# Optimization experiments

Measured on AMD Instinct MI355X. Metric: run time of the kernel, lower is better.

Reference implementation:

```python
import jax, jax.numpy as jnp
import numpy as np

N = 50000          # nodes
E = 600000         # edges
D_IN = 256         # input_feat_dim
H1 = 128           # hidden_dim1
H2 = 64            # hidden_dim2
DK = 64            # trs_depth (total key/value depth)
HEADS = 2


def setup_inputs() -> dict:
    key = jax.random.key(0)
    ks = jax.random.split(key, 12)
    inp = {
        "ns_emb": jax.random.normal(ks[0], (N, D_IN), dtype=jnp.float32),
        "edge_rows": jax.random.randint(ks[1], (E,), 0, N, dtype=jnp.int32),
        "edge_cols": jax.random.randint(ks[2], (E,), 0, N, dtype=jnp.int32),
        "edge_vals": jax.random.uniform(ks[3], (E,), dtype=jnp.float32),
        "condition": jax.random.normal(ks[4], (1, 128, H1), dtype=jnp.float32),
        # GCN linear weights (bias=False), stored [in, out]
        "W_hidden": jax.random.normal(ks[5], (D_IN, H1), dtype=jnp.float32) / np.sqrt(D_IN),
        "W_mu": jax.random.normal(ks[6], (H1, H2), dtype=jnp.float32) / np.sqrt(H1),
        "W_var": jax.random.normal(ks[7], (H1, H2), dtype=jnp.float32) / np.sqrt(H1),
        # MultiHeadAttention (bias-free) projections
        "Wq": jax.random.normal(ks[8], (H1, DK), dtype=jnp.float32) / np.sqrt(H1),
        "Wk": jax.random.normal(ks[9], (H1, DK), dtype=jnp.float32) / np.sqrt(H1),
        "Wv": jax.random.normal(ks[10], (H1, DK), dtype=jnp.float32) / np.sqrt(H1),
        "Wo": jax.random.normal(ks[11], (DK, H1), dtype=jnp.float32) / np.sqrt(DK),
    }
    return inp


def _spmm(rows, cols, vals, x):
    # sparse [N,N] @ x  via gather + segment-sum over COO edges
    gathered = vals[:, None] * x[cols]            # [E, d]
    return jax.ops.segment_sum(gathered, rows, num_segments=N)


def _gcn(x, W, rows, cols, vals):
    # dropout is identity in eval mode
    support = jax.nn.leaky_relu(x @ W)            # [N, out]
    out = _spmm(rows, cols, vals, support)        # [N, out]
    return jax.nn.leaky_relu(out)


def _mha(q, kv, Wq, Wk, Wv, Wo):
    # MoEL-style MultiHeadAttention, bias-free, no mask/dropout
    B, Lq, _ = q.shape
    Lk = kv.shape[1]
    dk = DK // HEADS
    Q = (q @ Wq).reshape(B, Lq, HEADS, dk).transpose(0, 2, 1, 3) * (dk ** -0.5)
    K = (kv @ Wk).reshape(B, Lk, HEADS, dk).transpose(0, 2, 1, 3)
    V = (kv @ Wv).reshape(B, Lk, HEADS, dk).transpose(0, 2, 1, 3)
    logits = jnp.einsum("bhqd,bhkd->bhqk", Q, K)
    w = jax.nn.softmax(logits, axis=-1)
    ctx = jnp.einsum("bhqk,bhkd->bhqd", w, V)
    ctx = ctx.transpose(0, 2, 1, 3).reshape(B, Lq, DK)
    return ctx @ Wo, w


def reference(ns_emb, edge_rows, edge_cols, edge_vals, condition,
              W_hidden, W_mu, W_var, Wq, Wk, Wv, Wo):
    hidden = _gcn(ns_emb, W_hidden, edge_rows, edge_cols, edge_vals)   # [N, H1]
    attended, _ = _mha(hidden[None], condition, Wq, Wk, Wv, Wo)        # [1, N, H1]
    h = attended[0]
    mu = _gcn(h, W_mu, edge_rows, edge_cols, edge_vals)                # [N, H2]
    var = _gcn(h, W_var, edge_rows, edge_cols, edge_vals)              # [N, H2]
    return mu, var
```

## Files before the change

### kernel.cpp

```cpp
#include <hip/hip_runtime.h>
#include <hip/hip_bf16.h>
#include <cstdint>


typedef __attribute__((ext_vector_type(8))) short short8;
typedef __attribute__((ext_vector_type(4))) float f32x4;
typedef __attribute__((ext_vector_type(4))) unsigned short ushort4_t;

__device__ __forceinline__ unsigned short f2bf(float f) {
    unsigned int u = __builtin_bit_cast(unsigned int, f);
    u += 0x7fffu + ((u >> 16) & 1u);
    return (unsigned short)(u >> 16);
}
__device__ __forceinline__ float bf2f(unsigned short v) {
    return __builtin_bit_cast(float, (unsigned int)v << 16);
}


__global__ void hist_kernel(const int* __restrict__ rows, int* __restrict__ cnt, int E) {
    int i = blockIdx.x * blockDim.x + threadIdx.x;
    if (i < E) atomicAdd(&cnt[rows[i]], 1);
}

__global__ void scan1_kernel(const int* __restrict__ cnt, int* __restrict__ excl,
                             int* __restrict__ bsum, int N) {
    __shared__ int sh[256];
    int t = threadIdx.x;
    int i = blockIdx.x * 256 + t;
    int v = (i < N) ? cnt[i] : 0;
    sh[t] = v;
    __syncthreads();
    for (int off = 1; off < 256; off <<= 1) {
        int x = (t >= off) ? sh[t - off] : 0;
        __syncthreads();
        sh[t] += x;
        __syncthreads();
    }
    if (i < N) excl[i] = sh[t] - v;
    if (t == 255) bsum[blockIdx.x] = sh[255];
}

__global__ void scan23_kernel(const int* __restrict__ excl, const int* __restrict__ bsum,
                              int* __restrict__ row_start, int* __restrict__ cursor,
                              int nb, int N, int E) {
    __shared__ int sh[256];
    int t = threadIdx.x;
    int v = (t < nb) ? bsum[t] : 0;
    sh[t] = v;
    __syncthreads();
    for (int off = 1; off < 256; off <<= 1) {
        int x = (t >= off) ? sh[t - off] : 0;
        __syncthreads();
        sh[t] += x;
        __syncthreads();
    }
    int boff = (blockIdx.x > 0) ? sh[blockIdx.x - 1] : 0;
    int i = blockIdx.x * 256 + t;
    if (i < N) {
        int w = excl[i] + boff;
        row_start[i] = w;
        cursor[i] = w;
    }
    if (i == 0) row_start[N] = E;
}

__global__ void scatter_kernel(const int* __restrict__ rows, const int* __restrict__ colsIn,
                               const float* __restrict__ valsIn, int* __restrict__ cursor,
                               int2* __restrict__ pack, int E) {
    int i = blockIdx.x * blockDim.x + threadIdx.x;
    if (i < E) {
        int r = rows[i];
        int p = atomicAdd(&cursor[r], 1);
        pack[p] = make_int2(colsIn[i], __float_as_int(valsIn[i]));
    }
}


__global__ __launch_bounds__(256) void prep_kv_kernel(
    const float* __restrict__ Wh, const float* __restrict__ Wq,
    const float* __restrict__ cond,
    const float* __restrict__ Wk, const float* __restrict__ Wv,
    const float* __restrict__ Wo, const float* __restrict__ Wmu,
    const float* __restrict__ Wvar,
    unsigned short* __restrict__ WhT, unsigned short* __restrict__ WqT,
    unsigned short* __restrict__ Ktt, unsigned short* __restrict__ Vt,
    unsigned short* __restrict__ WomT)
{
    const int t = threadIdx.x;
    const int bid = blockIdx.x;
    if (bid < 160) {
        int idx = bid * 256 + t;
        if (idx < 32768) {
            int n = idx & 127, k = idx >> 7;
            WhT[n * 256 + k] = f2bf(Wh[k * 128 + n]);
        } else {
            int i = idx - 32768, n = i & 63, k = i >> 6;
            WqT[n * 128 + k] = f2bf(Wq[k * 64 + n]);
        }
    } else if (bid < 224) {
        int b2 = bid - 160;
        __shared__ float c[2][128];
        c[t >> 7][t & 127] = cond[b2 * 256 + t];
        __syncthreads();
        int j = b2 * 2 + (t >> 7);
        int tl = t & 127;
        const float* W = (tl < 64) ? Wk : Wv;
        int col = tl & 63;
        float acc = 0.f;
#pragma unroll 8
        for (int k = 0; k < 128; ++k) acc = fmaf(c[t >> 7][k], W[k * 64 + col], acc);
        int h = col >> 5, d = col & 31;
        if (tl < 64) Ktt[((size_t)h * 128 + j) * 32 + d] = f2bf(acc * 0.17677669529663687f);
        else         Vt[((size_t)h * 32 + d) * 128 + j] = f2bf(acc);
    } else {
        int wb = bid - 224;
        __shared__ float WoTl[128 * 65];
#pragma unroll
        for (int i = 0; i < 32; ++i) {
            int idx = t + 256 * i;
            int d = idx >> 7, k = idx & 127;
            WoTl[k * 65 + d] = Wo[idx];
        }
        __syncthreads();
        int o = wb * 256 + t;
        int d = o & 63, n = o >> 6;
        const float* W = (n < 64) ? Wmu : Wvar;
        int j = n & 63;
        float acc = 0.f;
#pragma unroll 8
        for (int k = 0; k < 128; ++k) acc = fmaf(WoTl[k * 65 + d], W[k * 64 + j], acc);
        WomT[n * 64 + d] = f2bf(acc);
    }
}


__global__ __launch_bounds__(256) void gcn1_gemm(
    const float* __restrict__ A, const unsigned short* __restrict__ BT,
    unsigned short* __restrict__ C, int M)
{
    __shared__ unsigned short As[128][72];
    __shared__ unsigned short Bs[128][72];

    const int tid = threadIdx.x;
    const int lane = tid & 63, wave = tid >> 6;
    const int wm = wave & 1, wn = wave >> 1;
    const int quad = lane >> 4, l16 = lane & 15;
    const int r0 = blockIdx.x * 128;

    f32x4 acc[4][4];
#pragma unroll
    for (int mt = 0; mt < 4; ++mt)
#pragma unroll
        for (int nt = 0; nt < 4; ++nt)
#pragma unroll
            for (int r = 0; r < 4; ++r) acc[mt][nt][r] = 0.f;

    for (int kc = 0; kc < 256; kc += 64) {
#pragma unroll
        for (int i = 0; i < 8; ++i) {
            int f = tid + 256 * i;
            int row = f >> 4, kq = (f & 15) << 2;
            int gr = r0 + row;
            if (gr >= M) gr = M - 1;
            float4 v = *reinterpret_cast<const float4*>(&A[(size_t)gr * 256 + kc + kq]);
            unsigned int lo, hi;
            asm("v_cvt_pk_bf16_f32 %0, %1, %2" : "=v"(lo) : "v"(v.x), "v"(v.y));
            asm("v_cvt_pk_bf16_f32 %0, %1, %2" : "=v"(hi) : "v"(v.z), "v"(v.w));
            *reinterpret_cast<uint2*>(&As[row][kq]) = make_uint2(lo, hi);
        }
#pragma unroll
        for (int i = 0; i < 4; ++i) {
            int f = tid + 256 * i;
            int n = f >> 3, k8 = (f & 7) << 3;
            *reinterpret_cast<short8*>(&Bs[n][k8]) =
                *reinterpret_cast<const short8*>(&BT[(size_t)n * 256 + kc + k8]);
        }
        __syncthreads();

#pragma unroll
        for (int ks = 0; ks < 2; ++ks) {
            const int koff = ks * 32 + quad * 8;
            short8 a[4], b[4];
#pragma unroll
            for (int mt = 0; mt < 4; ++mt)
                a[mt] = *reinterpret_cast<const short8*>(&As[wm * 64 + mt * 16 + l16][koff]);
#pragma unroll
            for (int nt = 0; nt < 4; ++nt)
                b[nt] = *reinterpret_cast<const short8*>(&Bs[wn * 64 + nt * 16 + l16][koff]);
#pragma unroll
            for (int mt = 0; mt < 4; ++mt)
#pragma unroll
                for (int nt = 0; nt < 4; ++nt)
                    acc[mt][nt] = __builtin_amdgcn_mfma_f32_16x16x32_bf16(
                        a[mt], b[nt], acc[mt][nt], 0, 0, 0);
        }
        __syncthreads();
    }

#pragma unroll
    for (int mt = 0; mt < 4; ++mt)
#pragma unroll
        for (int nt = 0; nt < 4; ++nt) {
            int gc = wn * 64 + nt * 16 + l16;
#pragma unroll
            for (int r = 0; r < 4; ++r) {
                int gr = r0 + wm * 64 + mt * 16 + quad * 4 + r;
                if (gr < M) {
                    float v = acc[mt][nt][r];
                    v = v > 0.f ? v : 0.01f * v;
                    C[(size_t)gr * 128 + gc] = f2bf(v);
                }
            }
        }
}


__global__ __launch_bounds__(256) void attn_muvar_kernel(
    const unsigned short* __restrict__ hidden,
    const unsigned short* __restrict__ WqT,
    const unsigned short* __restrict__ Ktt,
    const unsigned short* __restrict__ Vt,
    const unsigned short* __restrict__ WomT,
    unsigned short* __restrict__ muvar,
    int M)
{
    __shared__ unsigned short Ap[64 * 136];
    __shared__ unsigned short Bp[10240];
    __shared__ unsigned short Cp[64 * 72];
    __shared__ float redm[2][64];
    __shared__ float reds[2][64];

    const int tid = threadIdx.x;
    const int lane = tid & 63, wave = tid >> 6;
    const int wm = wave & 1, wn = wave >> 1;
    const int quad = lane >> 4, l16 = lane & 15;
    const int r0 = blockIdx.x * 64;

#pragma unroll
    for (int i = 0; i < 4; ++i) {
        int f = tid + 256 * i;
        int row = f >> 4, k8 = (f & 15) << 3;
        int gr = r0 + row;
        if (gr >= M) gr = M - 1;
        *reinterpret_cast<short8*>(&Ap[row * 136 + k8]) =
            *reinterpret_cast<const short8*>(&hidden[(size_t)gr * 128 + k8]);
    }
#pragma unroll
    for (int i = 0; i < 4; ++i) {
        int f = tid + 256 * i;
        int n = f >> 4, k8 = (f & 15) << 3;
        *reinterpret_cast<short8*>(&Bp[n * 136 + k8]) =
            *reinterpret_cast<const short8*>(&WqT[(size_t)n * 128 + k8]);
    }
    __syncthreads();

    {
        f32x4 accq[2][2];
#pragma unroll
        for (int mt = 0; mt < 2; ++mt)
#pragma unroll
            for (int nt = 0; nt < 2; ++nt)
#pragma unroll
                for (int r = 0; r < 4; ++r) accq[mt][nt][r] = 0.f;
#pragma unroll
        for (int ks = 0; ks < 4; ++ks) {
            const int koff = ks * 32 + quad * 8;
            short8 a[2], b[2];
#pragma unroll
            for (int mt = 0; mt < 2; ++mt)
                a[mt] = *reinterpret_cast<const short8*>(&Ap[(wm * 32 + mt * 16 + l16) * 136 + koff]);
#pragma unroll
            for (int nt = 0; nt < 2; ++nt)
                b[nt] = *reinterpret_cast<const short8*>(&Bp[(wn * 32 + nt * 16 + l16) * 136 + koff]);
#pragma unroll
            for (int mt = 0; mt < 2; ++mt)
#pragma unroll
                for (int nt = 0; nt < 2; ++nt)
                    accq[mt][nt] = __builtin_amdgcn_mfma_f32_16x16x32_bf16(
                        a[mt], b[nt], accq[mt][nt], 0, 0, 0);
        }
#pragma unroll
        for (int mt = 0; mt < 2; ++mt)
#pragma unroll
            for (int nt = 0; nt < 2; ++nt) {
                int col = wn * 32 + nt * 16 + l16;
#pragma unroll
                for (int r = 0; r < 4; ++r) {
                    int row = wm * 32 + mt * 16 + quad * 4 + r;
                    Cp[row * 72 + col] = f2bf(accq[mt][nt][r]);
                }
            }
    }
    __syncthreads();

    for (int h = 0; h < 2; ++h) {
#pragma unroll
        for (int i = 0; i < 2; ++i) {
            int f = tid + 256 * i;
            int key = f >> 2, d8 = (f & 3) << 3;
            *reinterpret_cast<short8*>(&Bp[key * 40 + d8]) =
                *reinterpret_cast<const short8*>(&Ktt[((size_t)h * 128 + key) * 32 + d8]);
        }
#pragma unroll
        for (int i = 0; i < 2; ++i) {
            int f = tid + 256 * i;
            int d = f >> 4, k8 = (f & 15) << 3;
            *reinterpret_cast<short8*>(&Bp[5120 + d * 136 + k8]) =
                *reinterpret_cast<const short8*>(&Vt[((size_t)h * 32 + d) * 128 + k8]);
        }
        __syncthreads();

        f32x4 accl[2][4];
        {
            short8 a[2], b[4];
#pragma unroll
            for (int mt = 0; mt < 2; ++mt)
                a[mt] = *reinterpret_cast<const short8*>(&Cp[(wm * 32 + mt * 16 + l16) * 72 + h * 32 + quad * 8]);
#pragma unroll
            for (int nt = 0; nt < 4; ++nt)
                b[nt] = *reinterpret_cast<const short8*>(&Bp[(wn * 64 + nt * 16 + l16) * 40 + quad * 8]);
#pragma unroll
            for (int mt = 0; mt < 2; ++mt)
#pragma unroll
                for (int nt = 0; nt < 4; ++nt) {
                    f32x4 z; z[0] = 0.f; z[1] = 0.f; z[2] = 0.f; z[3] = 0.f;
                    accl[mt][nt] = __builtin_amdgcn_mfma_f32_16x16x32_bf16(a[mt], b[nt], z, 0, 0, 0);
                }
        }

#pragma unroll
        for (int mt = 0; mt < 2; ++mt)
#pragma unroll
            for (int r = 0; r < 4; ++r) {
                float mx = fmaxf(fmaxf(accl[mt][0][r], accl[mt][1][r]),
                                 fmaxf(accl[mt][2][r], accl[mt][3][r]));
#pragma unroll
                for (int off = 1; off < 16; off <<= 1)
                    mx = fmaxf(mx, __shfl_xor(mx, off, 64));
                if (l16 == 0) redm[wn][wm * 32 + mt * 16 + quad * 4 + r] = mx;
            }
        __syncthreads();
#pragma unroll
        for (int mt = 0; mt < 2; ++mt)
#pragma unroll
            for (int r = 0; r < 4; ++r) {
                int lr = wm * 32 + mt * 16 + quad * 4 + r;
                float fm = fmaxf(redm[0][lr], redm[1][lr]);
                float s = 0.f;
#pragma unroll
                for (int nt = 0; nt < 4; ++nt) {
                    float e = __expf(accl[mt][nt][r] - fm);
                    accl[mt][nt][r] = e;
                    s += e;
                }
#pragma unroll
                for (int off = 1; off < 16; off <<= 1)
                    s += __shfl_xor(s, off, 64);
                if (l16 == 0) reds[wn][lr] = s;
            }
        __syncthreads();
#pragma unroll
        for (int mt = 0; mt < 2; ++mt)
#pragma unroll
            for (int r = 0; r < 4; ++r) {
                int lr = wm * 32 + mt * 16 + quad * 4 + r;
                float inv = 1.0f / (reds[0][lr] + reds[1][lr]);
#pragma unroll
                for (int nt = 0; nt < 4; ++nt)
                    Ap[lr * 136 + wn * 64 + nt * 16 + l16] = f2bf(accl[mt][nt][r] * inv);
            }
        __syncthreads();

        {
            f32x4 accc[2];
#pragma unroll
            for (int mt = 0; mt < 2; ++mt)
#pragma unroll
                for (int r = 0; r < 4; ++r) accc[mt][r] = 0.f;
#pragma unroll
            for (int ks = 0; ks < 4; ++ks) {
                const int koff = ks * 32 + quad * 8;
                short8 a[2];
#pragma unroll
                for (int mt = 0; mt < 2; ++mt)
                    a[mt] = *reinterpret_cast<const short8*>(&Ap[(wm * 32 + mt * 16 + l16) * 136 + koff]);
                short8 bb = *reinterpret_cast<const short8*>(&Bp[5120 + (wn * 16 + l16) * 136 + koff]);
#pragma unroll
                for (int mt = 0; mt < 2; ++mt)
                    accc[mt] = __builtin_amdgcn_mfma_f32_16x16x32_bf16(a[mt], bb, accc[mt], 0, 0, 0);
            }
#pragma unroll
            for (int mt = 0; mt < 2; ++mt)
#pragma unroll
                for (int r = 0; r < 4; ++r) {
                    int row = wm * 32 + mt * 16 + quad * 4 + r;
                    Cp[row * 72 + h * 32 + wn * 16 + l16] = f2bf(accc[mt][r]);
                }
        }
        __syncthreads();
    }

#pragma unroll
    for (int i = 0; i < 4; ++i) {
        int f = tid + 256 * i;
        int n = f >> 3, k8 = (f & 7) << 3;
        *reinterpret_cast<short8*>(&Bp[n * 72 + k8]) =
            *reinterpret_cast<const short8*>(&WomT[(size_t)n * 64 + k8]);
    }
    __syncthreads();
    {
        f32x4 accf[2][4];
#pragma unroll
        for (int mt = 0; mt < 2; ++mt)
#pragma unroll
            for (int nt = 0; nt < 4; ++nt)
#pragma unroll
                for (int r = 0; r < 4; ++r) accf[mt][nt][r] = 0.f;
#pragma unroll
        for (int ks = 0; ks < 2; ++ks) {
            const int koff = ks * 32 + quad * 8;
            short8 a[2], b[4];
#pragma unroll
            for (int mt = 0; mt < 2; ++mt)
                a[mt] = *reinterpret_cast<const short8*>(&Cp[(wm * 32 + mt * 16 + l16) * 72 + koff]);
#pragma unroll
            for (int nt = 0; nt < 4; ++nt)
                b[nt] = *reinterpret_cast<const short8*>(&Bp[(wn * 64 + nt * 16 + l16) * 72 + koff]);
#pragma unroll
            for (int mt = 0; mt < 2; ++mt)
#pragma unroll
                for (int nt = 0; nt < 4; ++nt)
                    accf[mt][nt] = __builtin_amdgcn_mfma_f32_16x16x32_bf16(
                        a[mt], b[nt], accf[mt][nt], 0, 0, 0);
        }
#pragma unroll
        for (int mt = 0; mt < 2; ++mt)
#pragma unroll
            for (int nt = 0; nt < 4; ++nt) {
                int gc = wn * 64 + nt * 16 + l16;
#pragma unroll
                for (int r = 0; r < 4; ++r) {
                    int gr = r0 + wm * 32 + mt * 16 + quad * 4 + r;
                    if (gr < M) {
                        float v = accf[mt][nt][r];
                        v = v > 0.f ? v : 0.01f * v;
                        muvar[(size_t)gr * 128 + gc] = f2bf(v);
                    }
                }
            }
    }
}


template<bool SPLIT, typename OT>
__global__ __launch_bounds__(256) void spmm_kernel(
    const int* __restrict__ row_start, const int2* __restrict__ pack,
    const unsigned short* __restrict__ X,
    OT* __restrict__ out0, OT* __restrict__ out1, int N)
{
    const int wave = threadIdx.x >> 6, lane = threadIdx.x & 63;
    const int r = blockIdx.x * 4 + wave;
    if (r >= N) return;
    int s = __builtin_amdgcn_readfirstlane(row_start[r]);
    int e = __builtin_amdgcn_readfirstlane(row_start[r + 1]);
    const int fo = lane * 2;

    float ax[8], ay[8];
#pragma unroll
    for (int k = 0; k < 8; ++k) { ax[k] = 0.f; ay[k] = 0.f; }

    int i = s;
    for (; i + 8 <= e; i += 8) {
        int2 p[8];
        unsigned int x[8];
#pragma unroll
        for (int k = 0; k < 8; ++k) p[k] = pack[i + k];
#pragma unroll
        for (int k = 0; k < 8; ++k)
            x[k] = *reinterpret_cast<const unsigned int*>(&X[(size_t)p[k].x * 128 + fo]);
#pragma unroll
        for (int k = 0; k < 8; ++k) {
            float v = __int_as_float(p[k].y);
            ax[k] = fmaf(v, bf2f((unsigned short)x[k]), ax[k]);
            ay[k] = fmaf(v, bf2f((unsigned short)(x[k] >> 16)), ay[k]);
        }
    }
    if (i < e) {
        int2 p[8];
        unsigned int x[8];
#pragma unroll
        for (int k = 0; k < 8; ++k) {
            int idx = i + k;
            p[k] = pack[idx < e ? idx : e - 1];
        }
#pragma unroll
        for (int k = 0; k < 8; ++k)
            x[k] = *reinterpret_cast<const unsigned int*>(&X[(size_t)p[k].x * 128 + fo]);
#pragma unroll
        for (int k = 0; k < 8; ++k) {
            float v = (i + k < e) ? __int_as_float(p[k].y) : 0.f;
            ax[k] = fmaf(v, bf2f((unsigned short)x[k]), ax[k]);
            ay[k] = fmaf(v, bf2f((unsigned short)(x[k] >> 16)), ay[k]);
        }
    }

    float ox = ((ax[0] + ax[1]) + (ax[2] + ax[3])) + ((ax[4] + ax[5]) + (ax[6] + ax[7]));
    float oy = ((ay[0] + ay[1]) + (ay[2] + ay[3])) + ((ay[4] + ay[5]) + (ay[6] + ay[7]));
    ox = ox > 0.f ? ox : 0.01f * ox;
    oy = oy > 0.f ? oy : 0.01f * oy;

    if constexpr (!SPLIT) {
        unsigned int w = (unsigned int)f2bf(ox) | ((unsigned int)f2bf(oy) << 16);
        *reinterpret_cast<unsigned int*>(&out0[(size_t)r * 128 + fo]) = w;
    } else {
        if (lane < 32) {
            *reinterpret_cast<float2*>(&out0[(size_t)r * 64 + fo]) = make_float2(ox, oy);
        } else {
            *reinterpret_cast<float2*>(&out1[(size_t)r * 64 + (fo - 64)]) = make_float2(ox, oy);
        }
    }
}


extern "C" void kernel_launch(void* const* d_in, const int* in_sizes, int n_in,
                              void* d_out, int out_size, void* d_ws, size_t ws_size,
                              hipStream_t stream)
{
    const float* ns_emb   = (const float*)d_in[0];
    const int*   erows    = (const int*)d_in[1];
    const int*   ecols    = (const int*)d_in[2];
    const float* evals    = (const float*)d_in[3];
    const float* cond     = (const float*)d_in[4];
    const float* W_hidden = (const float*)d_in[5];
    const float* W_mu     = (const float*)d_in[6];
    const float* W_var    = (const float*)d_in[7];
    const float* Wq       = (const float*)d_in[8];
    const float* Wk       = (const float*)d_in[9];
    const float* Wv       = (const float*)d_in[10];
    const float* Wo       = (const float*)d_in[11];

    const int N = in_sizes[0] / 256;
    const int E = in_sizes[1];

    typedef unsigned short bf16;
    uint8_t* p = (uint8_t*)d_ws;
    auto alloc = [&](size_t bytes) {
        uint8_t* r = p;
        p += (bytes + 255) & ~(size_t)255;
        return r;
    };
    bf16* support1 = (bf16*)alloc(sizeof(bf16) * (size_t)N * 128);
    bf16* hidden   = (bf16*)alloc(sizeof(bf16) * (size_t)N * 128);
    bf16* muvarb   = (bf16*)alloc(sizeof(bf16) * (size_t)N * 128);
    bf16* Ktt      = (bf16*)alloc(sizeof(bf16) * 2 * 128 * 32);
    bf16* Vt       = (bf16*)alloc(sizeof(bf16) * 2 * 32 * 128);
    bf16* WhT      = (bf16*)alloc(sizeof(bf16) * 128 * 256);
    bf16* WqT      = (bf16*)alloc(sizeof(bf16) * 64 * 128);
    bf16* WomT     = (bf16*)alloc(sizeof(bf16) * 128 * 64);
    int*  cnt      = (int*)alloc(sizeof(int) * N);
    int*  excl     = (int*)alloc(sizeof(int) * N);
    int*  bsum     = (int*)alloc(sizeof(int) * 256);
    int*  row_start= (int*)alloc(sizeof(int) * (N + 1));
    int*  cursor   = (int*)alloc(sizeof(int) * N);
    int2* pack     = (int2*)alloc(sizeof(int2) * E);

    hipMemsetAsync(cnt, 0, sizeof(int) * N, stream);
    hist_kernel<<<(E + 255) / 256, 256, 0, stream>>>(erows, cnt, E);
    int nb = (N + 255) / 256;
    scan1_kernel<<<nb, 256, 0, stream>>>(cnt, excl, bsum, N);
    scan23_kernel<<<nb, 256, 0, stream>>>(excl, bsum, row_start, cursor, nb, N, E);
    scatter_kernel<<<(E + 255) / 256, 256, 0, stream>>>(erows, ecols, evals, cursor, pack, E);

    prep_kv_kernel<<<256, 256, 0, stream>>>(W_hidden, Wq, cond, Wk, Wv,
                                            Wo, W_mu, W_var,
                                            WhT, WqT, Ktt, Vt, WomT);

    const int mb128 = (N + 127) / 128;
    const int mb64  = (N + 63) / 64;
    const int sblocks = (N + 3) / 4;

    gcn1_gemm<<<mb128, 256, 0, stream>>>(ns_emb, WhT, support1, N);
    spmm_kernel<false, bf16><<<sblocks, 256, 0, stream>>>(
        row_start, pack, support1, hidden, nullptr, N);

    attn_muvar_kernel<<<mb64, 256, 0, stream>>>(hidden, WqT, Ktt, Vt,
                                                WomT, muvarb, N);

    float* out = (float*)d_out;
    spmm_kernel<true, float><<<sblocks, 256, 0, stream>>>(
        row_start, pack, muvarb, out, out + (size_t)N * 64, N);
}
```

Baseline: 268.8 us.

## Restructure attention kernel so each wave owns a 16-row strip without block barriers

The attention+mu/var kernel is rewritten so each wave independently handles 16 query rows. It computes Q, the full 128-key softmax and context in registers using the transposed MFMA orientation, then applies the output projection, using only per-wave LDS scratch. This removes the block-wide __syncthreads, the cross-wave softmax reductions and the cooperative LDS staging of weights. The cost is that weights (WqT, Ktt, Vt, WomT) are now read directly from global/L2 by every wave instead of being shared through LDS.

```diff
diff --git a/kernel.cpp b/kernel.cpp
--- a/kernel.cpp
+++ b/kernel.cpp
@@ -14,6 +14,11 @@
 }
 __device__ __forceinline__ float bf2f(unsigned short v) {
     return __builtin_bit_cast(float, (unsigned int)v << 16);
+}
+__device__ __forceinline__ unsigned int pk2(float a, float b) {
+    unsigned int r;
+    asm("v_cvt_pk_bf16_f32 %0, %1, %2" : "=v"(r) : "v"(a), "v"(b));
+    return r;
 }
 
 
@@ -163,9 +168,7 @@
             int gr = r0 + row;
             if (gr >= M) gr = M - 1;
             float4 v = *reinterpret_cast<const float4*>(&A[(size_t)gr * 256 + kc + kq]);
-            unsigned int lo, hi;
-            asm("v_cvt_pk_bf16_f32 %0, %1, %2" : "=v"(lo) : "v"(v.x), "v"(v.y));
-            asm("v_cvt_pk_bf16_f32 %0, %1, %2" : "=v"(hi) : "v"(v.z), "v"(v.w));
+            unsigned int lo = pk2(v.x, v.y), hi = pk2(v.z, v.w);
             *reinterpret_cast<uint2*>(&As[row][kq]) = make_uint2(lo, hi);
         }
 #pragma unroll
@@ -224,230 +227,156 @@
     unsigned short* __restrict__ muvar,
     int M)
 {
-    __shared__ unsigned short Ap[64 * 136];
-    __shared__ unsigned short Bp[10240];
-    __shared__ unsigned short Cp[64 * 72];
-    __shared__ float redm[2][64];
-    __shared__ float reds[2][64];
+    __shared__ unsigned short Qs[4][16 * 72];
+    __shared__ unsigned short Ps[4][16 * 136];
+    __shared__ unsigned short Csh[4][16 * 72];
 
     const int tid = threadIdx.x;
     const int lane = tid & 63, wave = tid >> 6;
-    const int wm = wave & 1, wn = wave >> 1;
     const int quad = lane >> 4, l16 = lane & 15;
-    const int r0 = blockIdx.x * 64;
-
-#pragma unroll
-    for (int i = 0; i < 4; ++i) {
-        int f = tid + 256 * i;
-        int row = f >> 4, k8 = (f & 15) << 3;
-        int gr = r0 + row;
-        if (gr >= M) gr = M - 1;
-        *reinterpret_cast<short8*>(&Ap[row * 136 + k8]) =
-            *reinterpret_cast<const short8*>(&hidden[(size_t)gr * 128 + k8]);
-    }
-#pragma unroll
-    for (int i = 0; i < 4; ++i) {
-        int f = tid + 256 * i;
-        int n = f >> 4, k8 = (f & 15) << 3;
-        *reinterpret_cast<short8*>(&Bp[n * 136 + k8]) =
-            *reinterpret_cast<const short8*>(&WqT[(size_t)n * 128 + k8]);
-    }
-    __syncthreads();
+
+    const int strip = blockIdx.x * 4 + wave;
+    const int base = strip * 16;
+    if (base >= M) return;
+    int qrow = base + l16;
+    if (qrow >= M) qrow = M - 1;
+
+    unsigned short* Q  = &Qs[wave][0];
+    unsigned short* P  = &Ps[wave][0];
+    unsigned short* Cl = &Csh[wave][0];
 
     {
-        f32x4 accq[2][2];
+        f32x4 qacc[4];
+#pragma unroll
+        for (int mt = 0; mt < 4; ++mt)
+#pragma unroll
+            for (int r = 0; r < 4; ++r) qacc[mt][r] = 0.f;
+
+        short8 hb[4];
+#pragma unroll
+        for (int ks = 0; ks < 4; ++ks)
+            hb[ks] = *reinterpret_cast<const short8*>(
+                &hidden[(size_t)qrow * 128 + ks * 32 + quad * 8]);
+#pragma unroll
+        for (int mt = 0; mt < 4; ++mt)
+#pragma unroll
+            for (int ks = 0; ks < 4; ++ks) {
+                short8 a = *reinterpret_cast<const short8*>(
+                    &WqT[(size_t)(mt * 16 + l16) * 128 + ks * 32 + quad * 8]);
+                qacc[mt] = __builtin_amdgcn_mfma_f32_16x16x32_bf16(a, hb[ks], qacc[mt], 0, 0, 0);
+            }
+#pragma unroll
+        for (int mt = 0; mt < 4; ++mt) {
+            uint2 w;
+            w.x = pk2(qacc[mt][0], qacc[mt][1]);
+            w.y = pk2(qacc[mt][2], qacc[mt][3]);
+            *reinterpret_cast<uint2*>(&Q[l16 * 72 + mt * 16 + quad * 4]) = w;
+        }
+    }
+
+    f32x4 ctv[2][2];
+#pragma unroll
+    for (int h = 0; h < 2; ++h)
 #pragma unroll
         for (int mt = 0; mt < 2; ++mt)
 #pragma unroll
-            for (int nt = 0; nt < 2; ++nt)
-#pragma unroll
-                for (int r = 0; r < 4; ++r) accq[mt][nt][r] = 0.f;
+            for (int r = 0; r < 4; ++r) ctv[h][mt][r] = 0.f;
+
+#pragma unroll
+    for (int h = 0; h < 2; ++h) {
+        f32x4 st[8];
+        short8 qb = *reinterpret_cast<const short8*>(&Q[l16 * 72 + h * 32 + quad * 8]);
+#pragma unroll
+        for (int mt = 0; mt < 8; ++mt) {
+            short8 a = *reinterpret_cast<const short8*>(
+                &Ktt[(size_t)h * 4096 + (mt * 16 + l16) * 32 + quad * 8]);
+            f32x4 z; z[0] = 0.f; z[1] = 0.f; z[2] = 0.f; z[3] = 0.f;
+            st[mt] = __builtin_amdgcn_mfma_f32_16x16x32_bf16(a, qb, z, 0, 0, 0);
+        }
+
+        float mx = st[0][0];
+#pragma unroll
+        for (int mt = 0; mt < 8; ++mt)
+#pragma unroll
+            for (int r = 0; r < 4; ++r) mx = fmaxf(mx, st[mt][r]);
+        mx = fmaxf(mx, __shfl_xor(mx, 16, 64));
+        mx = fmaxf(mx, __shfl_xor(mx, 32, 64));
+        float s = 0.f;
+#pragma unroll
+        for (int mt = 0; mt < 8; ++mt)
+#pragma unroll
+            for (int r = 0; r < 4; ++r) {
+                float e = __expf(st[mt][r] - mx);
+                st[mt][r] = e;
+                s += e;
+            }
+        s += __shfl_xor(s, 16, 64);
+        s += __shfl_xor(s, 32, 64);
+        float inv = 1.0f / s;
+
+#pragma unroll
+        for (int mt = 0; mt < 8; ++mt) {
+            uint2 w;
+            w.x = pk2(st[mt][0] * inv, st[mt][1] * inv);
+            w.y = pk2(st[mt][2] * inv, st[mt][3] * inv);
+            *reinterpret_cast<uint2*>(&P[l16 * 136 + mt * 16 + quad * 4]) = w;
+        }
+
 #pragma unroll
         for (int ks = 0; ks < 4; ++ks) {
-            const int koff = ks * 32 + quad * 8;
-            short8 a[2], b[2];
-#pragma unroll
-            for (int mt = 0; mt < 2; ++mt)
-                a[mt] = *reinterpret_cast<const short8*>(&Ap[(wm * 32 + mt * 16 + l16) * 136 + koff]);
-#pragma unroll
-            for (int nt = 0; nt < 2; ++nt)
-                b[nt] = *reinterpret_cast<const short8*>(&Bp[(wn * 32 + nt * 16 + l16) * 136 + koff]);
-#pragma unroll
-            for (int mt = 0; mt < 2; ++mt)
-#pragma unroll
-                for (int nt = 0; nt < 2; ++nt)
-                    accq[mt][nt] = __builtin_amdgcn_mfma_f32_16x16x32_bf16(
-                        a[mt], b[nt], accq[mt][nt], 0, 0, 0);
-        }
-#pragma unroll
-        for (int mt = 0; mt < 2; ++mt)
-#pragma unroll
-            for (int nt = 0; nt < 2; ++nt) {
-                int col = wn * 32 + nt * 16 + l16;
-#pragma unroll
-                for (int r = 0; r < 4; ++r) {
-                    int row = wm * 32 + mt * 16 + quad * 4 + r;
-                    Cp[row * 72 + col] = f2bf(accq[mt][nt][r]);
-                }
+            short8 pb = *reinterpret_cast<const short8*>(&P[l16 * 136 + ks * 32 + quad * 8]);
+#pragma unroll
+            for (int mt = 0; mt < 2; ++mt) {
+                short8 a = *reinterpret_cast<const short8*>(
+                    &Vt[(size_t)h * 4096 + (mt * 16 + l16) * 128 + ks * 32 + quad * 8]);
+                ctv[h][mt] = __builtin_amdgcn_mfma_f32_16x16x32_bf16(a, pb, ctv[h][mt], 0, 0, 0);
             }
-    }
-    __syncthreads();
-
-    for (int h = 0; h < 2; ++h) {
-#pragma unroll
-        for (int i = 0; i < 2; ++i) {
-            int f = tid + 256 * i;
-            int key = f >> 2, d8 = (f & 3) << 3;
-            *reinterpret_cast<short8*>(&Bp[key * 40 + d8]) =
-                *reinterpret_cast<const short8*>(&Ktt[((size_t)h * 128 + key) * 32 + d8]);
-        }
-#pragma unroll
-        for (int i = 0; i < 2; ++i) {
-            int f = tid + 256 * i;
-            int d = f >> 4, k8 = (f & 15) << 3;
-            *reinterpret_cast<short8*>(&Bp[5120 + d * 136 + k8]) =
-                *reinterpret_cast<const short8*>(&Vt[((size_t)h * 32 + d) * 128 + k8]);
-        }
-        __syncthreads();
-
-        f32x4 accl[2][4];
-        {
-            short8 a[2], b[4];
-#pragma unroll
-            for (int mt = 0; mt < 2; ++mt)
-                a[mt] = *reinterpret_cast<const short8*>(&Cp[(wm * 32 + mt * 16 + l16) * 72 + h * 32 + quad * 8]);
-#pragma unroll
-            for (int nt = 0; nt < 4; ++nt)
-                b[nt] = *reinterpret_cast<const short8*>(&Bp[(wn * 64 + nt * 16 + l16) * 40 + quad * 8]);
-#pragma unroll
-            for (int mt = 0; mt < 2; ++mt)
-#pragma unroll
-                for (int nt = 0; nt < 4; ++nt) {
-                    f32x4 z; z[0] = 0.f; z[1] = 0.f; z[2] = 0.f; z[3] = 0.f;
-                    accl[mt][nt] = __builtin_amdgcn_mfma_f32_16x16x32_bf16(a[mt], b[nt], z, 0, 0, 0);
-                }
-        }
-
-#pragma unroll
-        for (int mt = 0; mt < 2; ++mt)
-#pragma unroll
-            for (int r = 0; r < 4; ++r) {
-                float mx = fmaxf(fmaxf(accl[mt][0][r], accl[mt][1][r]),
-                                 fmaxf(accl[mt][2][r], accl[mt][3][r]));
-#pragma unroll
-                for (int off = 1; off < 16; off <<= 1)
-                    mx = fmaxf(mx, __shfl_xor(mx, off, 64));
-                if (l16 == 0) redm[wn][wm * 32 + mt * 16 + quad * 4 + r] = mx;
+        }
+    }
+
+#pragma unroll
+    for (int h = 0; h < 2; ++h)
+#pragma unroll
+        for (int mt = 0; mt < 2; ++mt) {
+            uint2 w;
+            w.x = pk2(ctv[h][mt][0], ctv[h][mt][1]);
+            w.y = pk2(ctv[h][mt][2], ctv[h][mt][3]);
+            *reinterpret_cast<uint2*>(&Cl[l16 * 72 + h * 32 + mt * 16 + quad * 4]) = w;
+        }
+
+    {
+        f32x4 mv[8];
+#pragma unroll
+        for (int mt = 0; mt < 8; ++mt)
+#pragma unroll
+            for (int r = 0; r < 4; ++r) mv[mt][r] = 0.f;
+        short8 cb[2];
+#pragma unroll
+        for (int ks = 0; ks < 2; ++ks)
+            cb[ks] = *reinterpret_cast<const short8*>(&Cl[l16 * 72 + ks * 32 + quad * 8]);
+#pragma unroll
+        for (int mt = 0; mt < 8; ++mt)
+#pragma unroll
+            for (int ks = 0; ks < 2; ++ks) {
+                short8 a = *reinterpret_cast<const short8*>(
+                    &WomT[(size_t)(mt * 16 + l16) * 64 + ks * 32 + quad * 8]);
+                mv[mt] = __builtin_amdgcn_mfma_f32_16x16x32_bf16(a, cb[ks], mv[mt], 0, 0, 0);
             }
-        __syncthreads();
-#pragma unroll
-        for (int mt = 0; mt < 2; ++mt)
-#pragma unroll
-            for (int r = 0; r < 4; ++r) {
-                int lr = wm * 32 + mt * 16 + quad * 4 + r;
-                float fm = fmaxf(redm[0][lr], redm[1][lr]);
-                float s = 0.f;
-#pragma unroll
-                for (int nt = 0; nt < 4; ++nt) {
-                    float e = __expf(accl[mt][nt][r] - fm);
-                    accl[mt][nt][r] = e;
-                    s += e;
-                }
-#pragma unroll
-                for (int off = 1; off < 16; off <<= 1)
-                    s += __shfl_xor(s, off, 64);
-                if (l16 == 0) reds[wn][lr] = s;
+        if (base + l16 < M) {
+#pragma unroll
+            for (int mt = 0; mt < 8; ++mt) {
+                float v0 = mv[mt][0], v1 = mv[mt][1], v2 = mv[mt][2], v3 = mv[mt][3];
+                v0 = v0 > 0.f ? v0 : 0.01f * v0;
+                v1 = v1 > 0.f ? v1 : 0.01f * v1;
+                v2 = v2 > 0.f ? v2 : 0.01f * v2;
+                v3 = v3 > 0.f ? v3 : 0.01f * v3;
+                uint2 w;
+                w.x = pk2(v0, v1);
+                w.y = pk2(v2, v3);
+                *reinterpret_cast<uint2*>(
+                    &muvar[(size_t)(base + l16) * 128 + mt * 16 + quad * 4]) = w;
             }
-        __syncthreads();
-#pragma unroll
-        for (int mt = 0; mt < 2; ++mt)
-#pragma unroll
-            for (int r = 0; r < 4; ++r) {
-                int lr = wm * 32 + mt * 16 + quad * 4 + r;
-                float inv = 1.0f / (reds[0][lr] + reds[1][lr]);
-#pragma unroll
-                for (int nt = 0; nt < 4; ++nt)
-                    Ap[lr * 136 + wn * 64 + nt * 16 + l16] = f2bf(accl[mt][nt][r] * inv);
-            }
-        __syncthreads();
-
-        {
-            f32x4 accc[2];
-#pragma unroll
-            for (int mt = 0; mt < 2; ++mt)
-#pragma unroll
-                for (int r = 0; r < 4; ++r) accc[mt][r] = 0.f;
-#pragma unroll
-            for (int ks = 0; ks < 4; ++ks) {
-                const int koff = ks * 32 + quad * 8;
-                short8 a[2];
-#pragma unroll
-                for (int mt = 0; mt < 2; ++mt)
-                    a[mt] = *reinterpret_cast<const short8*>(&Ap[(wm * 32 + mt * 16 + l16) * 136 + koff]);
-                short8 bb = *reinterpret_cast<const short8*>(&Bp[5120 + (wn * 16 + l16) * 136 + koff]);
-#pragma unroll
-                for (int mt = 0; mt < 2; ++mt)
-                    accc[mt] = __builtin_amdgcn_mfma_f32_16x16x32_bf16(a[mt], bb, accc[mt], 0, 0, 0);
-            }
-#pragma unroll
-            for (int mt = 0; mt < 2; ++mt)
-#pragma unroll
-                for (int r = 0; r < 4; ++r) {
-                    int row = wm * 32 + mt * 16 + quad * 4 + r;
-                    Cp[row * 72 + h * 32 + wn * 16 + l16] = f2bf(accc[mt][r]);
-                }
-        }
-        __syncthreads();
-    }
-
-#pragma unroll
-    for (int i = 0; i < 4; ++i) {
-        int f = tid + 256 * i;
-        int n = f >> 3, k8 = (f & 7) << 3;
-        *reinterpret_cast<short8*>(&Bp[n * 72 + k8]) =
-            *reinterpret_cast<const short8*>(&WomT[(size_t)n * 64 + k8]);
-    }
-    __syncthreads();
-    {
-        f32x4 accf[2][4];
-#pragma unroll
-        for (int mt = 0; mt < 2; ++mt)
-#pragma unroll
-            for (int nt = 0; nt < 4; ++nt)
-#pragma unroll
-                for (int r = 0; r < 4; ++r) accf[mt][nt][r] = 0.f;
-#pragma unroll
-        for (int ks = 0; ks < 2; ++ks) {
-            const int koff = ks * 32 + quad * 8;
-            short8 a[2], b[4];
-#pragma unroll
-            for (int mt = 0; mt < 2; ++mt)
-                a[mt] = *reinterpret_cast<const short8*>(&Cp[(wm * 32 + mt * 16 + l16) * 72 + koff]);
-#pragma unroll
-            for (int nt = 0; nt < 4; ++nt)
-                b[nt] = *reinterpret_cast<const short8*>(&Bp[(wn * 64 + nt * 16 + l16) * 72 + koff]);
-#pragma unroll
-            for (int mt = 0; mt < 2; ++mt)
-#pragma unroll
-                for (int nt = 0; nt < 4; ++nt)
-                    accf[mt][nt] = __builtin_amdgcn_mfma_f32_16x16x32_bf16(
-                        a[mt], b[nt], accf[mt][nt], 0, 0, 0);
-        }
-#pragma unroll
-        for (int mt = 0; mt < 2; ++mt)
-#pragma unroll
-            for (int nt = 0; nt < 4; ++nt) {
-                int gc = wn * 64 + nt * 16 + l16;
-#pragma unroll
-                for (int r = 0; r < 4; ++r) {
-                    int gr = r0 + wm * 32 + mt * 16 + quad * 4 + r;
-                    if (gr < M) {
-                        float v = accf[mt][nt][r];
-                        v = v > 0.f ? v : 0.01f * v;
-                        muvar[(size_t)gr * 128 + gc] = f2bf(v);
-                    }
-                }
-            }
+        }
     }
 }
 
@@ -576,15 +505,16 @@
                                             WhT, WqT, Ktt, Vt, WomT);
 
     const int mb128 = (N + 127) / 128;
-    const int mb64  = (N + 63) / 64;
+    const int strips = (N + 15) / 16;
+    const int ablocks = (strips + 3) / 4;
     const int sblocks = (N + 3) / 4;
 
     gcn1_gemm<<<mb128, 256, 0, stream>>>(ns_emb, WhT, support1, N);
     spmm_kernel<false, bf16><<<sblocks, 256, 0, stream>>>(
         row_start, pack, support1, hidden, nullptr, N);
 
-    attn_muvar_kernel<<<mb64, 256, 0, stream>>>(hidden, WqT, Ktt, Vt,
-                                                WomT, muvarb, N);
+    attn_muvar_kernel<<<ablocks, 256, 0, stream>>>(hidden, WqT, Ktt, Vt,
+                                                   WomT, muvarb, N);
 
     float* out = (float*)d_out;
     spmm_kernel<true, float><<<sblocks, 256, 0, stream>>>(
```

Measured after the change: 270.2 us. Within noise of the previous version (+0.5%).
